# Kernel tuning notes

Hardware: AMD Instinct MI355X
Metric: run time of the kernel (lower is better)

Reference implementation:

```python
import jax, jax.numpy as jnp
import numpy as np

RADIUS = 2                 # soft detection radius (init kwarg)
NMS_RADIUS = 2             # hardcoded in detect_keypoints: simple_nms(scores, 2)
TOP_K = 4096
TEMPERATURE = 0.1
KSIZE = 2 * RADIUS + 1     # 5
KK = KSIZE * KSIZE         # 25


def _hw_grid(dtype):
    # flatten order j = dy*KSIZE + dx ; entry = (x_off, y_off)  (torch's [:, [1,0]])
    lin = jnp.linspace(-RADIUS, RADIUS, KSIZE, dtype=dtype)
    gx, gy = jnp.meshgrid(lin, lin)  # 'xy': gx[dy,dx]=lin[dx], gy[dy,dx]=lin[dy]
    return jnp.stack([gx, gy], axis=-1).reshape(-1, 2)  # (KK, 2)


def _maxpool(x, r):
    k = 2 * r + 1
    return jax.lax.reduce_window(x, -jnp.inf, jax.lax.max,
                                 (1, 1, k, k), (1, 1, 1, 1),
                                 ((0, 0), (0, 0), (r, r), (r, r)))


def _simple_nms(scores, r):
    zeros = jnp.zeros_like(scores)
    max_mask = scores == _maxpool(scores, r)
    for _ in range(2):
        supp_mask = _maxpool(max_mask.astype(scores.dtype), r) > 0
        supp_scores = jnp.where(supp_mask, zeros, scores)
        new_max_mask = supp_scores == _maxpool(supp_scores, r)
        max_mask = max_mask | (new_max_mask & ~supp_mask)
    return jnp.where(max_mask, scores, zeros)


def _bilinear_zeros(img, xy):
    # img: (h, w); xy: (K, 2) normalized [-1,1]; align_corners=True, zero padding
    h, w = img.shape
    px = (xy[:, 0] + 1.0) * 0.5 * (w - 1)
    py = (xy[:, 1] + 1.0) * 0.5 * (h - 1)
    x0 = jnp.floor(px); y0 = jnp.floor(py)
    wx1 = px - x0; wx0 = 1.0 - wx1
    wy1 = py - y0; wy0 = 1.0 - wy1
    def tap(xi, yi, wgt):
        valid = (xi >= 0) & (xi < w) & (yi >= 0) & (yi < h)
        xc = jnp.clip(xi, 0, w - 1).astype(jnp.int32)
        yc = jnp.clip(yi, 0, h - 1).astype(jnp.int32)
        return jnp.where(valid, img[yc, xc], 0.0) * wgt
    return (tap(x0, y0, wx0 * wy0) + tap(x0 + 1, y0, wx1 * wy0)
            + tap(x0, y0 + 1, wx0 * wy1) + tap(x0 + 1, y0 + 1, wx1 * wy1))


def _dkd_forward(scores_map):
    b, c, h, w = scores_map.shape
    dtype = scores_map.dtype
    scores_nograd = jax.lax.stop_gradient(scores_map)

    nms_scores = _simple_nms(scores_nograd, NMS_RADIUS)
    # zero out border band of width RADIUS
    ybad = (jnp.arange(h) < RADIUS) | (jnp.arange(h) >= h - RADIUS)
    xbad = (jnp.arange(w) < RADIUS) | (jnp.arange(w) >= w - RADIUS)
    border = ybad[:, None] | xbad[None, :]
    nms_scores = jnp.where(border[None, None], 0.0, nms_scores)

    # top-k over flattened score map (per image)
    _, idx = jax.lax.top_k(nms_scores.reshape(b, -1), TOP_K)  # (b, K)
    ix = idx % w
    iy = idx // w

    # patch gather == unfold(scores_map) + gather, done sparsely with zero pad
    padded = jnp.pad(scores_map[:, 0], ((0, 0), (RADIUS, RADIUS), (RADIUS, RADIUS)))
    off = jnp.arange(KSIZE)
    ys = iy[:, :, None] + off[None, None, :]           # (b, K, KSIZE)
    xs = ix[:, :, None] + off[None, None, :]
    bidx = jnp.arange(b)[:, None, None, None]
    patch_scores = padded[bidx, ys[:, :, :, None], xs[:, :, None, :]]  # (b,K,KSIZE,KSIZE)
    patch_scores = patch_scores.reshape(b, TOP_K, KK)

    hw_grid = _hw_grid(dtype)                          # (KK, 2)
    max_v = jax.lax.stop_gradient(patch_scores.max(axis=-1, keepdims=True))
    x_exp = jnp.exp((patch_scores - max_v) / TEMPERATURE)   # (b,K,KK)
    x_exp_sum = x_exp.sum(axis=-1, keepdims=True)            # (b,K,1)
    xy_residual = jnp.einsum('bkp,pd->bkd', x_exp, hw_grid) / x_exp_sum  # (b,K,2)
    hw_dist2 = (((hw_grid[None, None] - xy_residual[:, :, None]) / RADIUS) ** 2).sum(-1)
    scoredispersity = (x_exp * hw_dist2).sum(-1) / x_exp_sum[..., 0]     # (b,K)

    keypoints_xy_nms = jnp.stack([ix, iy], axis=-1).astype(dtype)
    wh = jnp.array([w - 1, h - 1], dtype=dtype)
    keypoints_xy = (keypoints_xy_nms + xy_residual) / wh * 2.0 - 1.0     # (b,K,2)

    kptscore = jax.vmap(_bilinear_zeros)(scores_map[:, 0], keypoints_xy)  # (b,K)
    return keypoints_xy, kptscore, scoredispersity


def setup_inputs() -> dict:
    key = jax.random.key(0)
    scores_map = jax.random.uniform(key, (8, 1, 1024, 1024), dtype=jnp.float32)
    return {"scores_map": scores_map}


def reference(scores_map):
    # matches torch forward: (keypoints, kptscores, scoredispersitys)
    return _dkd_forward(scores_map)
```

## Files before the change

### kernel.cpp

```cpp
#include <hip/hip_runtime.h>
#include <stdint.h>

namespace {

constexpr int B = 8;
constexpr int H = 1024;
constexpr int W = 1024;
constexpr int TOPK = 4096;
constexpr int CAND_CAP = 131072;
constexpr int SEL_CAP = 16384;
constexpr int LIST_CAP = 320;

constexpr int HIST_BINS = 3840;
constexpr int HIST_BASE = 112 << 8;

constexpr int RROWS = 78;
constexpr int NG = 20;
constexpr int STR = 80;
constexpr int MW = 5;
constexpr int NSM = 9;
constexpr int NSE = 8;
constexpr int NUNIT_M = NG * NSM;
constexpr int NUNIT_E = NG * NSE;

constexpr int RK_ME = 256;
constexpr int RK_CH = 1024;

constexpr size_t OFF_CNT   = 0;
constexpr size_t OFF_GH    = 4096;
constexpr size_t OFF_RANK  = OFF_GH + (size_t)B * HIST_BINS * 4;
constexpr size_t OFF_SEL   = OFF_RANK + (size_t)B * SEL_CAP * 4;
constexpr size_t OFF_CAND  = OFF_SEL + (size_t)B * SEL_CAP * 8;
constexpr size_t MEMSET_BYTES = OFF_RANK;

__device__ __forceinline__ float max5(float a, float b, float c, float d, float e) {
  return fmaxf(fmaxf(fmaxf(a, b), fmaxf(c, d)), e);
}
__device__ __forceinline__ float4 ld4(const float* p) {
  return *reinterpret_cast<const float4*>(p);
}

template <int PASS>
__device__ __forceinline__ void score_pass(
    int u, int x0, int y0, const float* __restrict__ S,
    const uint32_t* __restrict__ MIN_, uint32_t* __restrict__ MOUT,
    uint64_t* list, uint32_t* cnt_loc, uint64_t* cand, uint32_t* cand_count,
    uint32_t* __restrict__ ghist, int b) {
  const int G = u % NG, s = u / NG;
  const int r0 = ((PASS == 2) ? 8 : 4) + 8 * s;
  const int gx0 = x0 - 8 + 4 * G;
  uint32_t colm = 0;
#pragma unroll
  for (int j = 0; j < 4; ++j)
    if ((unsigned)(gx0 + j) < (unsigned)W) colm |= 1u << j;

  const int p2 = 4 * G - 6;
  const int pw2 = (p2 < 0) ? 0 : (p2 >> 5);
  const int psh2 = (p2 < 0) ? 0 : (p2 & 31);
  const int pls2 = (p2 < 0) ? -p2 : 0;

  float4 hw[5], cw[5];
  uint32_t snr[5], mor[5], cnb[5];
  constexpr int NK = (PASS == 0) ? 12 : 16;
#pragma unroll
  for (int k = 0; k < NK; ++k) {
    if (PASS != 0) {
      const int mr = r0 - 4 + k;
      uint32_t morrow = 0, cnib = 0;
      if ((unsigned)mr < (unsigned)RROWS) {
        const uint32_t* srow = MIN_ + mr * MW;
        uint64_t X = (uint64_t)srow[pw2] | ((uint64_t)srow[pw2 + 1] << 32);
        uint64_t win = pls2 ? (X << pls2) : (X >> psh2);
        uint64_t t5 = win | (win >> 1) | (win >> 2) | (win >> 3) | (win >> 4);
        morrow = (uint32_t)t5 & 0xFFFu;
        cnib = (uint32_t)(win >> 6) & 0xFu;
      }
      mor[k % 5] = morrow;
      cnb[k % 5] = cnib;
    }
    const int ks = (PASS == 0) ? k : k - 4;
    if (ks >= 0) {
      const int sr = r0 - 2 + ks;
      uint32_t supp = 0;
      if (PASS != 0) supp = mor[0] | mor[1] | mor[2] | mor[3] | mor[4];
      const float* rowp = S + sr * STR + 4 * G;
      float4 d = ld4(rowp);
      float4 a = (G > 0) ? ld4(rowp - 4) : d;
      float4 e = (G < NG - 1) ? ld4(rowp + 4) : d;
      if (PASS != 0) {
        if (supp & 0x001u) a.x = 0.f;
        if (supp & 0x002u) a.y = 0.f;
        if (supp & 0x004u) a.z = 0.f;
        if (supp & 0x008u) a.w = 0.f;
        if (supp & 0x010u) d.x = 0.f;
        if (supp & 0x020u) d.y = 0.f;
        if (supp & 0x040u) d.z = 0.f;
        if (supp & 0x080u) d.w = 0.f;
        if (supp & 0x100u) e.x = 0.f;
        if (supp & 0x200u) e.y = 0.f;
        if (supp & 0x400u) e.z = 0.f;
        if (supp & 0x800u) e.w = 0.f;
      }
      float4 hm;
      hm.x = max5(a.z, a.w, d.x, d.y, d.z);
      hm.y = max5(a.w, d.x, d.y, d.z, d.w);
      hm.z = max5(d.x, d.y, d.z, d.w, e.x);
      hm.w = max5(d.y, d.z, d.w, e.x, e.y);
      hw[ks % 5] = hm;
      cw[ks % 5] = d;
      snr[ks % 5] = (supp >> 4) & 0xFu;
      if (ks >= 4) {
        const int rq = r0 - 4 + ks;
        const int gy = y0 - 8 + rq;
        float4 vm;
        vm.x = max5(hw[0].x, hw[1].x, hw[2].x, hw[3].x, hw[4].x);
        vm.y = max5(hw[0].y, hw[1].y, hw[2].y, hw[3].y, hw[4].y);
        vm.z = max5(hw[0].z, hw[1].z, hw[2].z, hw[3].z, hw[4].z);
        vm.w = max5(hw[0].w, hw[1].w, hw[2].w, hw[3].w, hw[4].w);
        float4 c = cw[(ks + 3) % 5];
        uint32_t nm = (uint32_t)(c.x == vm.x) | ((uint32_t)(c.y == vm.y) << 1) |
                      ((uint32_t)(c.z == vm.z) << 2) | ((uint32_t)(c.w == vm.w) << 3);
        nm &= ((unsigned)gy < (unsigned)H) ? colm : 0u;
        const int widx = rq * MW + (G >> 3);
        const int shift = 4 * (G & 7);
        if (PASS == 0) {
          if (nm) atomicOr(&MOUT[widx], nm << shift);
        } else if (PASS == 1) {
          uint32_t fin = cnb[ks % 5] | (nm & ~snr[(ks + 3) % 5]);
          if (fin) atomicOr(&MOUT[widx], fin << shift);
        } else {
          uint32_t fin = cnb[ks % 5] | (nm & ~snr[(ks + 3) % 5]);
          if (fin && G >= 2 && G < 18 && gy >= 2 && gy < H - 2) {
#pragma unroll
            for (int j = 0; j < 4; ++j) {
              if ((fin >> j) & 1u) {
                int gx = gx0 + j;
                if (gx >= 2 && gx < W - 2) {
                  float sval = S[rq * STR + 4 * G + j];
                  if (sval > 0.0f) {
                    uint32_t bits = __float_as_uint(sval);
                    uint32_t flat = (uint32_t)(gy * W + gx);
                    uint64_t key = ((uint64_t)bits << 32) | (uint64_t)(0xFFFFFFFFu - flat);
                    uint32_t pos = atomicAdd(cnt_loc, 1u);
                    if (pos < (uint32_t)LIST_CAP) {
                      list[pos] = key;
                    } else {
                      uint32_t pp = atomicAdd(&cand_count[b], 1u);
                      if (pp < (uint32_t)CAND_CAP) cand[(size_t)b * CAND_CAP + pp] = key;
                      int bin = (int)(bits >> 15) - HIST_BASE;
                      if (bin < 0) bin = 0;
                      if (bin >= HIST_BINS) bin = HIST_BINS - 1;
                      atomicAdd(&ghist[(size_t)b * HIST_BINS + bin], 1u);
                    }
                  }
                }
              }
            }
          }
        }
      }
    }
  }
}

__global__ void __launch_bounds__(256, 4) k_nms(const float* __restrict__ scores,
                                                uint64_t* __restrict__ cand,
                                                uint32_t* __restrict__ cand_count,
                                                uint32_t* __restrict__ ghist) {
  __shared__ float S[RROWS * STR];
  __shared__ uint32_t M0s[RROWS * MW];
  __shared__ uint32_t M1s[RROWS * MW];
  __shared__ uint64_t list[LIST_CAP];
  __shared__ uint32_t cnt_loc, base_g;
  const int b = blockIdx.z;
  const int x0 = blockIdx.x * 64, y0 = blockIdx.y * 64;
  const int tid = threadIdx.x;
  const float* img = scores + (size_t)b * H * W;
  if (tid == 0) cnt_loc = 0;

  for (int u = tid; u < RROWS * NG; u += 256) {
    int r = u / NG, G = u % NG;
    int gy = y0 - 8 + r, gx = x0 - 8 + 4 * G;
    float4 v;
    if ((unsigned)gy < (unsigned)H && (unsigned)gx < (unsigned)W)
      v = ld4(img + (size_t)gy * W + gx);
    else
      v = make_float4(-INFINITY, -INFINITY, -INFINITY, -INFINITY);
    *reinterpret_cast<float4*>(&S[r * STR + 4 * G]) = v;
  }
  for (int i = tid; i < RROWS * MW; i += 256) {
    M0s[i] = 0;
    M1s[i] = 0;
  }
  __syncthreads();
  if (tid < NUNIT_M)
    score_pass<0>(tid, x0, y0, S, nullptr, M0s, nullptr, nullptr, nullptr, nullptr,
                  nullptr, b);
  __syncthreads();
  if (tid < NUNIT_M)
    score_pass<1>(tid, x0, y0, S, M0s, M1s, nullptr, nullptr, nullptr, nullptr,
                  nullptr, b);
  __syncthreads();
  if (tid < NUNIT_E)
    score_pass<2>(tid, x0, y0, S, M1s, nullptr, list, &cnt_loc, cand, cand_count,
                  ghist, b);
  __syncthreads();
  uint32_t nblk = cnt_loc;
  uint32_t nmain = nblk < (uint32_t)LIST_CAP ? nblk : (uint32_t)LIST_CAP;
  if (tid == 0) base_g = atomicAdd(&cand_count[b], nmain);
  uint32_t* Shist = (uint32_t*)S;
  for (int i = tid; i < HIST_BINS; i += 256) Shist[i] = 0;
  __syncthreads();
  uint32_t bg = base_g;
  for (uint32_t i = tid; i < nmain; i += 256) {
    uint64_t key = list[i];
    uint32_t pp = bg + i;
    if (pp < (uint32_t)CAND_CAP) cand[(size_t)b * CAND_CAP + pp] = key;
    int bin = (int)(uint32_t)(key >> 47) - HIST_BASE;
    if (bin < 0) bin = 0;
    atomicAdd(&Shist[bin], 1u);
  }
  __syncthreads();
  for (int i = tid; i < HIST_BINS; i += 256) {
    uint32_t v = Shist[i];
    if (v) atomicAdd(&ghist[(size_t)b * HIST_BINS + i], v);
  }
}

__global__ void __launch_bounds__(1024) k_compact(const uint64_t* __restrict__ cand,
                                                  const uint32_t* __restrict__ cand_count,
                                                  const uint32_t* __restrict__ ghist,
                                                  uint64_t* __restrict__ sel,
                                                  uint32_t* __restrict__ sel_count,
                                                  uint32_t* __restrict__ rankg) {
  __shared__ uint64_t list[1024];
  __shared__ uint32_t cnt_loc, base_g;
  __shared__ uint32_t h[1024];
  __shared__ uint64_t s_thr;
  const int b = blockIdx.y;
  uint32_t n = cand_count[b];
  if (n > (uint32_t)CAND_CAP) n = CAND_CAP;
  if (blockIdx.x * 1024u >= n) return;
  const int tid = threadIdx.x;
  if (tid == 0) {
    cnt_loc = 0;
    s_thr = 0ull;
  }
  const uint32_t* gh = ghist + (size_t)b * HIST_BINS;
  uint4 mybins = make_uint4(0u, 0u, 0u, 0u);
  uint32_t s = 0;
  if (tid < HIST_BINS / 4) {
    mybins = reinterpret_cast<const uint4*>(gh)[tid];
    s = mybins.x + mybins.y + mybins.z + mybins.w;
  }
  h[tid] = s;
  __syncthreads();
  for (int d = 1; d < 1024; d <<= 1) {
    uint32_t v = (tid + d < 1024) ? h[tid + d] : 0u;
    __syncthreads();
    h[tid] += v;
    __syncthreads();
  }
  {
    uint32_t cum = h[tid];
    uint32_t nxt = (tid < 1023) ? h[tid + 1] : 0u;
    if (cum >= (uint32_t)TOPK && nxt < (uint32_t)TOPK) {
      uint32_t run = nxt;
      uint32_t binv[4] = {mybins.x, mybins.y, mybins.z, mybins.w};
      int thrbin = 4 * tid;
#pragma unroll
      for (int j = 3; j >= 0; --j) {
        run += binv[j];
        if (run >= (uint32_t)TOPK) {
          thrbin = 4 * tid + j;
          break;
        }
      }
      if (thrbin > 0)
        s_thr = ((uint64_t)(uint32_t)(thrbin + HIST_BASE)) << 47;
    }
  }
  __syncthreads();
  const uint64_t thr = s_thr;
  uint32_t i = blockIdx.x * 1024 + tid;
  if (i < n) {
    uint64_t key = cand[(size_t)b * CAND_CAP + i];
    if (key >= thr) {
      uint32_t pos = atomicAdd(&cnt_loc, 1u);
      list[pos] = key;
    }
  }
  __syncthreads();
  uint32_t nblk = cnt_loc;
  if (tid == 0 && nblk > 0) base_g = atomicAdd(&sel_count[b], nblk);
  __syncthreads();
  if (nblk > 0 && (uint32_t)tid < nblk) {
    uint32_t pp = base_g + tid;
    if (pp < (uint32_t)SEL_CAP) {
      sel[(size_t)b * SEL_CAP + pp] = list[tid];
      rankg[(size_t)b * SEL_CAP + pp] = 0u;
    }
  }
}

__global__ void __launch_bounds__(RK_ME) k_rank_part(const uint64_t* __restrict__ sel,
                                                     const uint32_t* __restrict__ sel_count,
                                                     uint32_t* __restrict__ rankg) {
  __shared__ uint64_t keys[RK_CH];
  const int b = blockIdx.z;
  uint32_t n = sel_count[b];
  if (n > (uint32_t)SEL_CAP) n = SEL_CAP;
  const uint32_t me0 = blockIdx.x * RK_ME;
  const uint32_t c0 = blockIdx.y * RK_CH;
  if (me0 >= n || c0 >= n) return;
  const uint64_t* sb = sel + (size_t)b * SEL_CAP;
  uint32_t clen = n - c0;
  if (clen > (uint32_t)RK_CH) clen = RK_CH;
  for (uint32_t i = threadIdx.x; i < clen; i += RK_ME) keys[i] = sb[c0 + i];
  __syncthreads();
  const uint32_t me = me0 + threadIdx.x;
  if (me >= n) return;
  const uint64_t kme = sb[me];
  uint32_t rank = 0;
  uint32_t i = 0;
  for (; i + 8 <= clen; i += 8) {
    rank += (keys[i] > kme);
    rank += (keys[i + 1] > kme);
    rank += (keys[i + 2] > kme);
    rank += (keys[i + 3] > kme);
    rank += (keys[i + 4] > kme);
    rank += (keys[i + 5] > kme);
    rank += (keys[i + 6] > kme);
    rank += (keys[i + 7] > kme);
  }
  for (; i < clen; ++i) rank += (keys[i] > kme);
  if (rank) atomicAdd(&rankg[(size_t)b * SEL_CAP + me], rank);
}

__global__ void __launch_bounds__(256) k_refine(const float* __restrict__ scores,
                                                const uint64_t* __restrict__ sel,
                                                const uint32_t* __restrict__ sel_count,
                                                const uint32_t* __restrict__ rankg,
                                                float* __restrict__ out) {
  int gid = blockIdx.x * 256 + threadIdx.x;
  int idx = gid >> 3, ln = gid & 7;
  const int b = idx / SEL_CAP;
  const int i = idx % SEL_CAP;
  uint32_t n = sel_count[b];
  if (n > (uint32_t)SEL_CAP) n = SEL_CAP;
  if ((uint32_t)i >= n) return;
  uint32_t r = rankg[(size_t)b * SEL_CAP + i];
  if (r >= (uint32_t)TOPK) return;
  uint64_t key = sel[(size_t)b * SEL_CAP + i];
  uint32_t flat = 0xFFFFFFFFu - (uint32_t)(key & 0xFFFFFFFFull);
  if (flat >= (uint32_t)(H * W)) flat = 0;
  const int ix = (int)(flat % W);
  const int iy = (int)(flat / W);
  const float* img = scores + (size_t)b * H * W;

  const int nt = (ln == 0) ? 4 : 3;
  float v[4];
  float mymax = -INFINITY;
#pragma unroll
  for (int q = 0; q < 4; ++q) {
    if (q < nt) {
      int t = ln + 8 * q;
      int y = iy + t / 5 - 2, x = ix + t % 5 - 2;
      float val = ((unsigned)x < (unsigned)W && (unsigned)y < (unsigned)H)
                      ? img[(size_t)y * W + x] : 0.0f;
      v[q] = val;
      mymax = fmaxf(mymax, val);
    }
  }
#pragma unroll
  for (int m = 1; m < 8; m <<= 1) mymax = fmaxf(mymax, __shfl_xor(mymax, m));
  float e[4];
  float sum = 0.f, sx = 0.f, sy = 0.f;
#pragma unroll
  for (int q = 0; q < 4; ++q) {
    if (q < nt) {
      int t = ln + 8 * q;
      float ev = expf((v[q] - mymax) / 0.1f);
      e[q] = ev;
      sum += ev;
      sx += ev * (float)(t % 5 - 2);
      sy += ev * (float)(t / 5 - 2);
    }
  }
#pragma unroll
  for (int m = 1; m < 8; m <<= 1) {
    sum += __shfl_xor(sum, m);
    sx += __shfl_xor(sx, m);
    sy += __shfl_xor(sy, m);
  }
  float rx = sx / sum, ry = sy / sum;
  float dsp = 0.f;
#pragma unroll
  for (int q = 0; q < 4; ++q) {
    if (q < nt) {
      int t = ln + 8 * q;
      float dx = ((float)(t % 5 - 2) - rx) * 0.5f;
      float dy = ((float)(t / 5 - 2) - ry) * 0.5f;
      dsp += e[q] * (dx * dx + dy * dy);
    }
  }
#pragma unroll
  for (int m = 1; m < 8; m <<= 1) dsp += __shfl_xor(dsp, m);
  if (ln != 0) return;
  dsp /= sum;
  float kx = ((float)ix + rx) / 1023.0f * 2.0f - 1.0f;
  float ky = ((float)iy + ry) / 1023.0f * 2.0f - 1.0f;
  float px = (kx + 1.0f) * 0.5f * 1023.0f;
  float py = (ky + 1.0f) * 0.5f * 1023.0f;
  float x0f = floorf(px), y0f = floorf(py);
  float wx1 = px - x0f, wx0 = 1.0f - wx1;
  float wy1 = py - y0f, wy0 = 1.0f - wy1;
  int x0 = (int)x0f, y0 = (int)y0f;
  float sc = 0.0f;
  {
    int xs[2] = {x0, x0 + 1};
    int ys[2] = {y0, y0 + 1};
    float wxs[2] = {wx0, wx1};
    float wys[2] = {wy0, wy1};
#pragma unroll
    for (int yy = 0; yy < 2; ++yy)
#pragma unroll
      for (int xx = 0; xx < 2; ++xx) {
        int xi = xs[xx], yi = ys[yy];
        bool valid = (xi >= 0 && xi < W && yi >= 0 && yi < H);
        int xc = min(max(xi, 0), W - 1);
        int yc = min(max(yi, 0), H - 1);
        float vv = valid ? img[(size_t)yc * W + xc] : 0.0f;
        sc += vv * (wxs[xx] * wys[yy]);
      }
  }
  out[((size_t)b * TOPK + r) * 2 + 0] = kx;
  out[((size_t)b * TOPK + r) * 2 + 1] = ky;
  out[(size_t)B * TOPK * 2 + (size_t)b * TOPK + r] = sc;
  out[(size_t)B * TOPK * 3 + (size_t)b * TOPK + r] = dsp;
}

}

extern "C" void kernel_launch(void* const* d_in, const int* in_sizes, int n_in,
                              void* d_out, int out_size, void* d_ws, size_t ws_size,
                              hipStream_t stream) {
  const float* scores = (const float*)d_in[0];
  float* out = (float*)d_out;
  char* ws = (char*)d_ws;

  uint32_t* cnt = (uint32_t*)(ws + OFF_CNT);
  uint32_t* cand_count = cnt;
  uint32_t* sel_count  = cnt + 8;
  uint32_t* ghist = (uint32_t*)(ws + OFF_GH);
  uint32_t* rankg = (uint32_t*)(ws + OFF_RANK);
  uint64_t* sel  = (uint64_t*)(ws + OFF_SEL);
  uint64_t* cand = (uint64_t*)(ws + OFF_CAND);

  hipMemsetAsync(ws + OFF_CNT, 0, MEMSET_BYTES, stream);

  k_nms<<<dim3(W / 64, H / 64, B), 256, 0, stream>>>(scores, cand, cand_count, ghist);
  k_compact<<<dim3(CAND_CAP / 1024, B), 1024, 0, stream>>>(cand, cand_count, ghist,
                                                           sel, sel_count, rankg);
  k_rank_part<<<dim3(SEL_CAP / RK_ME, SEL_CAP / RK_CH, B), RK_ME, 0, stream>>>(
      sel, sel_count, rankg);
  k_refine<<<(B * SEL_CAP * 8) / 256, 256, 0, stream>>>(scores, sel, sel_count, rankg,
                                                        out);
}
```

Measured before the change: 188.0 us.

## Fuse rank and refine kernels via last-block-done counter

Merges the partial-rank kernel and the refine kernel into one launch. Each member block increments a per-(batch, member-block) done counter after contributing its partial ranks. The last arriving chunk block then performs the soft-detection refinement for that block's 256 candidates, reading ranks atomically. This removes a kernel launch and the mostly-idle refine grid, at the cost of threadfences, atomics and serializing refinement into fewer blocks.

```diff
diff --git a/kernel.cpp b/kernel.cpp
--- a/kernel.cpp
+++ b/kernel.cpp
@@ -25,6 +25,8 @@
 
 constexpr int RK_ME = 256;
 constexpr int RK_CH = 1024;
+constexpr int NMB = SEL_CAP / RK_ME;
+constexpr int NCB = SEL_CAP / RK_CH;
 
 constexpr size_t OFF_CNT   = 0;
 constexpr size_t OFF_GH    = 4096;
@@ -303,141 +305,153 @@
   }
 }
 
-__global__ void __launch_bounds__(RK_ME) k_rank_part(const uint64_t* __restrict__ sel,
-                                                     const uint32_t* __restrict__ sel_count,
-                                                     uint32_t* __restrict__ rankg) {
+__global__ void __launch_bounds__(RK_ME) k_rankref(const float* __restrict__ scores,
+                                                   const uint64_t* __restrict__ sel,
+                                                   const uint32_t* __restrict__ sel_count,
+                                                   uint32_t* __restrict__ rankg,
+                                                   uint32_t* __restrict__ done,
+                                                   float* __restrict__ out) {
   __shared__ uint64_t keys[RK_CH];
+  __shared__ uint32_t s_old;
   const int b = blockIdx.z;
+  const int me_blk = blockIdx.x;
   uint32_t n = sel_count[b];
   if (n > (uint32_t)SEL_CAP) n = SEL_CAP;
-  const uint32_t me0 = blockIdx.x * RK_ME;
+  const uint32_t me0 = (uint32_t)me_blk * RK_ME;
+  if (me0 >= n) return;
   const uint32_t c0 = blockIdx.y * RK_CH;
-  if (me0 >= n || c0 >= n) return;
+  const int tid = threadIdx.x;
   const uint64_t* sb = sel + (size_t)b * SEL_CAP;
-  uint32_t clen = n - c0;
-  if (clen > (uint32_t)RK_CH) clen = RK_CH;
-  for (uint32_t i = threadIdx.x; i < clen; i += RK_ME) keys[i] = sb[c0 + i];
-  __syncthreads();
-  const uint32_t me = me0 + threadIdx.x;
-  if (me >= n) return;
-  const uint64_t kme = sb[me];
-  uint32_t rank = 0;
-  uint32_t i = 0;
-  for (; i + 8 <= clen; i += 8) {
-    rank += (keys[i] > kme);
-    rank += (keys[i + 1] > kme);
-    rank += (keys[i + 2] > kme);
-    rank += (keys[i + 3] > kme);
-    rank += (keys[i + 4] > kme);
-    rank += (keys[i + 5] > kme);
-    rank += (keys[i + 6] > kme);
-    rank += (keys[i + 7] > kme);
-  }
-  for (; i < clen; ++i) rank += (keys[i] > kme);
-  if (rank) atomicAdd(&rankg[(size_t)b * SEL_CAP + me], rank);
-}
-
-__global__ void __launch_bounds__(256) k_refine(const float* __restrict__ scores,
-                                                const uint64_t* __restrict__ sel,
-                                                const uint32_t* __restrict__ sel_count,
-                                                const uint32_t* __restrict__ rankg,
-                                                float* __restrict__ out) {
-  int gid = blockIdx.x * 256 + threadIdx.x;
-  int idx = gid >> 3, ln = gid & 7;
-  const int b = idx / SEL_CAP;
-  const int i = idx % SEL_CAP;
-  uint32_t n = sel_count[b];
-  if (n > (uint32_t)SEL_CAP) n = SEL_CAP;
-  if ((uint32_t)i >= n) return;
-  uint32_t r = rankg[(size_t)b * SEL_CAP + i];
-  if (r >= (uint32_t)TOPK) return;
-  uint64_t key = sel[(size_t)b * SEL_CAP + i];
-  uint32_t flat = 0xFFFFFFFFu - (uint32_t)(key & 0xFFFFFFFFull);
-  if (flat >= (uint32_t)(H * W)) flat = 0;
-  const int ix = (int)(flat % W);
-  const int iy = (int)(flat / W);
+
+  if (c0 < n) {
+    uint32_t clen = n - c0;
+    if (clen > (uint32_t)RK_CH) clen = RK_CH;
+    for (uint32_t i = tid; i < clen; i += RK_ME) keys[i] = sb[c0 + i];
+    __syncthreads();
+    const uint32_t me = me0 + tid;
+    if (me < n) {
+      const uint64_t kme = sb[me];
+      uint32_t rank = 0;
+      uint32_t i = 0;
+      for (; i + 8 <= clen; i += 8) {
+        rank += (keys[i] > kme);
+        rank += (keys[i + 1] > kme);
+        rank += (keys[i + 2] > kme);
+        rank += (keys[i + 3] > kme);
+        rank += (keys[i + 4] > kme);
+        rank += (keys[i + 5] > kme);
+        rank += (keys[i + 6] > kme);
+        rank += (keys[i + 7] > kme);
+      }
+      for (; i < clen; ++i) rank += (keys[i] > kme);
+      if (rank) atomicAdd(&rankg[(size_t)b * SEL_CAP + me], rank);
+    }
+  }
+  __syncthreads();
+  __threadfence();
+  if (tid == 0) s_old = atomicAdd(&done[b * NMB + me_blk], 1u);
+  __syncthreads();
+  if (s_old != (uint32_t)(NCB - 1)) return;
+  __threadfence();
+
+  const int ln = tid & 7;
+  const int lane = tid & 63;
   const float* img = scores + (size_t)b * H * W;
-
-  const int nt = (ln == 0) ? 4 : 3;
-  float v[4];
-  float mymax = -INFINITY;
-#pragma unroll
-  for (int q = 0; q < 4; ++q) {
-    if (q < nt) {
-      int t = ln + 8 * q;
-      int y = iy + t / 5 - 2, x = ix + t % 5 - 2;
-      float val = ((unsigned)x < (unsigned)W && (unsigned)y < (unsigned)H)
-                      ? img[(size_t)y * W + x] : 0.0f;
-      v[q] = val;
-      mymax = fmaxf(mymax, val);
-    }
-  }
-#pragma unroll
-  for (int m = 1; m < 8; m <<= 1) mymax = fmaxf(mymax, __shfl_xor(mymax, m));
-  float e[4];
-  float sum = 0.f, sx = 0.f, sy = 0.f;
-#pragma unroll
-  for (int q = 0; q < 4; ++q) {
-    if (q < nt) {
-      int t = ln + 8 * q;
-      float ev = expf((v[q] - mymax) / 0.1f);
-      e[q] = ev;
-      sum += ev;
-      sx += ev * (float)(t % 5 - 2);
-      sy += ev * (float)(t / 5 - 2);
-    }
-  }
-#pragma unroll
-  for (int m = 1; m < 8; m <<= 1) {
-    sum += __shfl_xor(sum, m);
-    sx += __shfl_xor(sx, m);
-    sy += __shfl_xor(sy, m);
-  }
-  float rx = sx / sum, ry = sy / sum;
-  float dsp = 0.f;
-#pragma unroll
-  for (int q = 0; q < 4; ++q) {
-    if (q < nt) {
-      int t = ln + 8 * q;
-      float dx = ((float)(t % 5 - 2) - rx) * 0.5f;
-      float dy = ((float)(t / 5 - 2) - ry) * 0.5f;
-      dsp += e[q] * (dx * dx + dy * dy);
-    }
-  }
-#pragma unroll
-  for (int m = 1; m < 8; m <<= 1) dsp += __shfl_xor(dsp, m);
-  if (ln != 0) return;
-  dsp /= sum;
-  float kx = ((float)ix + rx) / 1023.0f * 2.0f - 1.0f;
-  float ky = ((float)iy + ry) / 1023.0f * 2.0f - 1.0f;
-  float px = (kx + 1.0f) * 0.5f * 1023.0f;
-  float py = (ky + 1.0f) * 0.5f * 1023.0f;
-  float x0f = floorf(px), y0f = floorf(py);
-  float wx1 = px - x0f, wx0 = 1.0f - wx1;
-  float wy1 = py - y0f, wy0 = 1.0f - wy1;
-  int x0 = (int)x0f, y0 = (int)y0f;
-  float sc = 0.0f;
-  {
-    int xs[2] = {x0, x0 + 1};
-    int ys[2] = {y0, y0 + 1};
-    float wxs[2] = {wx0, wx1};
-    float wys[2] = {wy0, wy1};
-#pragma unroll
-    for (int yy = 0; yy < 2; ++yy)
-#pragma unroll
-      for (int xx = 0; xx < 2; ++xx) {
-        int xi = xs[xx], yi = ys[yy];
-        bool valid = (xi >= 0 && xi < W && yi >= 0 && yi < H);
-        int xc = min(max(xi, 0), W - 1);
-        int yc = min(max(yi, 0), H - 1);
-        float vv = valid ? img[(size_t)yc * W + xc] : 0.0f;
-        sc += vv * (wxs[xx] * wys[yy]);
-      }
-  }
-  out[((size_t)b * TOPK + r) * 2 + 0] = kx;
-  out[((size_t)b * TOPK + r) * 2 + 1] = ky;
-  out[(size_t)B * TOPK * 2 + (size_t)b * TOPK + r] = sc;
-  out[(size_t)B * TOPK * 3 + (size_t)b * TOPK + r] = dsp;
+#pragma unroll 1
+  for (int it = 0; it < RK_ME / 32; ++it) {
+    const uint32_t i = me0 + (uint32_t)(it * 32 + (tid >> 3));
+    if (i >= n) continue;
+    uint32_t r = 0;
+    if (ln == 0) r = atomicAdd(&rankg[(size_t)b * SEL_CAP + i], 0u);
+    r = (uint32_t)__shfl((int)r, lane & ~7);
+    if (r >= (uint32_t)TOPK) continue;
+    uint64_t key = sb[i];
+    uint32_t flat = 0xFFFFFFFFu - (uint32_t)(key & 0xFFFFFFFFull);
+    if (flat >= (uint32_t)(H * W)) flat = 0;
+    const int ix = (int)(flat % W);
+    const int iy = (int)(flat / W);
+
+    const int nt = (ln == 0) ? 4 : 3;
+    float v[4];
+    float mymax = -INFINITY;
+#pragma unroll
+    for (int q = 0; q < 4; ++q) {
+      if (q < nt) {
+        int t = ln + 8 * q;
+        int y = iy + t / 5 - 2, x = ix + t % 5 - 2;
+        float val = ((unsigned)x < (unsigned)W && (unsigned)y < (unsigned)H)
+                        ? img[(size_t)y * W + x] : 0.0f;
+        v[q] = val;
+        mymax = fmaxf(mymax, val);
+      }
+    }
+#pragma unroll
+    for (int m = 1; m < 8; m <<= 1) mymax = fmaxf(mymax, __shfl_xor(mymax, m));
+    float e[4];
+    float sum = 0.f, sx = 0.f, sy = 0.f;
+#pragma unroll
+    for (int q = 0; q < 4; ++q) {
+      if (q < nt) {
+        int t = ln + 8 * q;
+        float ev = expf((v[q] - mymax) / 0.1f);
+        e[q] = ev;
+        sum += ev;
+        sx += ev * (float)(t % 5 - 2);
+        sy += ev * (float)(t / 5 - 2);
+      }
+    }
+#pragma unroll
+    for (int m = 1; m < 8; m <<= 1) {
+      sum += __shfl_xor(sum, m);
+      sx += __shfl_xor(sx, m);
+      sy += __shfl_xor(sy, m);
+    }
+    float rx = sx / sum, ry = sy / sum;
+    float dsp = 0.f;
+#pragma unroll
+    for (int q = 0; q < 4; ++q) {
+      if (q < nt) {
+        int t = ln + 8 * q;
+        float dx = ((float)(t % 5 - 2) - rx) * 0.5f;
+        float dy = ((float)(t / 5 - 2) - ry) * 0.5f;
+        dsp += e[q] * (dx * dx + dy * dy);
+      }
+    }
+#pragma unroll
+    for (int m = 1; m < 8; m <<= 1) dsp += __shfl_xor(dsp, m);
+    if (ln != 0) continue;
+    dsp /= sum;
+    float kx = ((float)ix + rx) / 1023.0f * 2.0f - 1.0f;
+    float ky = ((float)iy + ry) / 1023.0f * 2.0f - 1.0f;
+    float px = (kx + 1.0f) * 0.5f * 1023.0f;
+    float py = (ky + 1.0f) * 0.5f * 1023.0f;
+    float x0f = floorf(px), y0f = floorf(py);
+    float wx1 = px - x0f, wx0 = 1.0f - wx1;
+    float wy1 = py - y0f, wy0 = 1.0f - wy1;
+    int x0 = (int)x0f, y0 = (int)y0f;
+    float sc = 0.0f;
+    {
+      int xs[2] = {x0, x0 + 1};
+      int ys[2] = {y0, y0 + 1};
+      float wxs[2] = {wx0, wx1};
+      float wys[2] = {wy0, wy1};
+#pragma unroll
+      for (int yy = 0; yy < 2; ++yy)
+#pragma unroll
+        for (int xx = 0; xx < 2; ++xx) {
+          int xi = xs[xx], yi = ys[yy];
+          bool valid = (xi >= 0 && xi < W && yi >= 0 && yi < H);
+          int xc = min(max(xi, 0), W - 1);
+          int yc = min(max(yi, 0), H - 1);
+          float vv = valid ? img[(size_t)yc * W + xc] : 0.0f;
+          sc += vv * (wxs[xx] * wys[yy]);
+        }
+    }
+    out[((size_t)b * TOPK + r) * 2 + 0] = kx;
+    out[((size_t)b * TOPK + r) * 2 + 1] = ky;
+    out[(size_t)B * TOPK * 2 + (size_t)b * TOPK + r] = sc;
+    out[(size_t)B * TOPK * 3 + (size_t)b * TOPK + r] = dsp;
+  }
 }
 
 }
@@ -452,6 +466,7 @@
   uint32_t* cnt = (uint32_t*)(ws + OFF_CNT);
   uint32_t* cand_count = cnt;
   uint32_t* sel_count  = cnt + 8;
+  uint32_t* done       = cnt + 256;
   uint32_t* ghist = (uint32_t*)(ws + OFF_GH);
   uint32_t* rankg = (uint32_t*)(ws + OFF_RANK);
   uint64_t* sel  = (uint64_t*)(ws + OFF_SEL);
@@ -462,8 +477,6 @@
   k_nms<<<dim3(W / 64, H / 64, B), 256, 0, stream>>>(scores, cand, cand_count, ghist);
   k_compact<<<dim3(CAND_CAP / 1024, B), 1024, 0, stream>>>(cand, cand_count, ghist,
                                                            sel, sel_count, rankg);
-  k_rank_part<<<dim3(SEL_CAP / RK_ME, SEL_CAP / RK_CH, B), RK_ME, 0, stream>>>(
-      sel, sel_count, rankg);
-  k_refine<<<(B * SEL_CAP * 8) / 256, 256, 0, stream>>>(scores, sel, sel_count, rankg,
-                                                        out);
-}
+  k_rankref<<<dim3(NMB, NCB, B), RK_ME, 0, stream>>>(scores, sel, sel_count, rankg,
+                                                     done, out);
+}
```

Result: slower. 370.3 us (+97.0%).
